# Optimization experiments

Measured on AMD Instinct MI355X. Metric: run time of the kernel, lower is better.

Reference implementation:

```python
import jax, jax.numpy as jnp
import numpy as np
from jax import lax

EPS = 1e-5  # torch LayerNorm / BatchNorm1d default eps
HEADS, DH, DEPTH, C = 4, 128, 2, 512


def setup_inputs() -> dict:
    key = jax.random.key(0)
    ks = iter(jax.random.split(key, 48))
    def rn(shape, scale=1.0):
        return jax.random.normal(next(ks), shape, jnp.float32) * scale
    d, L = 1024, DEPTH
    inp = {}
    inp['x'] = rn((16, 10, 256, d))                      # (b, ncrops, T, d)
    # Temporal embedding: Conv1d(d -> 512, k=3, pad=1) + ReLU
    inp['W_emb'] = rn((C, d, 3), (d * 3) ** -0.5)
    inp['b_emb'] = jnp.zeros((C,), jnp.float32)
    # Transformer (depth=2), params stacked along layer axis
    inp['ln1_g'] = jnp.ones((L, C), jnp.float32); inp['ln1_b'] = jnp.zeros((L, C), jnp.float32)
    inp['W_qkv'] = rn((L, C, 4 * HEADS * DH), C ** -0.5)  # to_qkv (no bias), inner_dim*4 = 2048
    inp['W_o']  = rn((L, 2 * HEADS * DH, C), (2 * HEADS * DH) ** -0.5)
    inp['b_o']  = jnp.zeros((L, C), jnp.float32)
    inp['ln2_g'] = jnp.ones((L, C), jnp.float32); inp['ln2_b'] = jnp.zeros((L, C), jnp.float32)
    inp['W_f1'] = rn((L, C, C), C ** -0.5); inp['b_f1'] = jnp.zeros((L, C), jnp.float32)
    inp['W_f2'] = rn((L, C, C), C ** -0.5); inp['b_f2'] = jnp.zeros((L, C), jnp.float32)
    # NormalHead: conv1 512->32 (k=1), bn1, conv2 32->16 (k=1), bn2, conv3 16->1 (k=1)
    inp['c1_W'] = rn((32, C), C ** -0.5); inp['c1_b'] = jnp.zeros((32,), jnp.float32)
    inp['bn1_g'] = jnp.ones((32,), jnp.float32); inp['bn1_b'] = jnp.zeros((32,), jnp.float32)
    inp['bn1_m'] = rn((32,), 0.1)
    inp['bn1_v'] = jax.random.uniform(next(ks), (32,), jnp.float32, 0.5, 1.5)
    inp['c2_W'] = rn((16, 32), 32 ** -0.5); inp['c2_b'] = jnp.zeros((16,), jnp.float32)
    inp['bn2_g'] = jnp.ones((16,), jnp.float32); inp['bn2_b'] = jnp.zeros((16,), jnp.float32)
    inp['bn2_m'] = rn((16,), 0.1)
    inp['bn2_v'] = jax.random.uniform(next(ks), (16,), jnp.float32, 0.5, 1.5)
    inp['c3_W'] = rn((1, 16), 0.25); inp['c3_b'] = jnp.zeros((1,), jnp.float32)
    return inp


def _ln(z, g, b):
    m = z.mean(-1, keepdims=True)
    v = ((z - m) ** 2).mean(-1, keepdims=True)
    return (z - m) / jnp.sqrt(v + EPS) * g + b


def _bn_eval(z, g, b, m, v):  # z: (B, C, T), eval-mode BatchNorm1d
    return (z - m[None, :, None]) / jnp.sqrt(v[None, :, None] + EPS) * g[None, :, None] + b[None, :, None]


def _k1conv(z, W, b):  # pointwise Conv1d: z (B, Ci, T), W (Co, Ci)
    return jnp.einsum('bct,oc->bot', z, W) + b[None, :, None]


def reference(x, W_emb, b_emb, ln1_g, ln1_b, W_qkv, W_o, b_o, ln2_g, ln2_b,
              W_f1, b_f1, W_f2, b_f2, c1_W, c1_b, bn1_g, bn1_b, bn1_m, bn1_v,
              c2_W, c2_b, bn2_g, bn2_b, bn2_m, bn2_v, c3_W, c3_b):
    b, n, T, d = x.shape
    h = x.reshape(b * n, T, d)
    # Temporal embedding: Conv1d(k=3, pad=1) + ReLU
    h = lax.conv_general_dilated(h.transpose(0, 2, 1), W_emb, (1,), 'SAME',
                                 dimension_numbers=('NCH', 'OIH', 'NCH'))
    h = jax.nn.relu(h + b_emb[None, :, None]).transpose(0, 2, 1)  # (BN, T, 512)

    # fixed positional-decay attention map attn2 (T, T), batch-independent
    idx = jnp.arange(T, dtype=jnp.float32)
    tg = jnp.abs(idx[None, :] - idx[:, None])
    a2 = jnp.exp(-tg / jnp.exp(1.0))
    a2 = a2 / a2.sum(-1)  # NOTE: broadcast over last axis, exactly as in the torch code

    scale = DH ** -0.5
    for l in range(DEPTH):
        z = _ln(h, ln1_g[l], ln1_b[l])
        qkvt = z @ W_qkv[l]                                   # (BN, T, 2048)
        q, k, v, t = jnp.split(qkvt, 4, axis=-1)
        def to_heads(u):
            return u.reshape(u.shape[0], T, HEADS, DH).transpose(0, 2, 1, 3)
        q, k, v, t = map(to_heads, (q, k, v, t))              # (BN, H, T, DH)
        attn1 = jax.nn.softmax(jnp.einsum('bhid,bhjd->bhij', q, k) * scale, axis=-1)
        o1 = jnp.einsum('bhij,bhjd->bhid', attn1, v)
        o2 = jnp.einsum('ij,bhjd->bhid', a2, t)
        o = jnp.concatenate([o1, o2], axis=-1)                # (BN, H, T, 2*DH)
        o = o.transpose(0, 2, 1, 3).reshape(h.shape[0], T, HEADS * 2 * DH)
        h = o @ W_o[l] + b_o[l] + h                           # attn residual
        z = _ln(h, ln2_g[l], ln2_b[l])
        h = (jax.nn.gelu(z @ W_f1[l] + b_f1[l], approximate=False) @ W_f2[l] + b_f2[l]) + h

    # NormalHead on (BN, C, T)
    f = h.transpose(0, 2, 1)
    x1 = _k1conv(f, c1_W, c1_b)                               # (BN, 32, T)
    x2 = _k1conv(jax.nn.relu(_bn_eval(x1, bn1_g, bn1_b, bn1_m, bn1_v)), c2_W, c2_b)  # (BN, 16, T)
    scores = jax.nn.sigmoid(_k1conv(jax.nn.relu(_bn_eval(x2, bn2_g, bn2_b, bn2_m, bn2_v)), c3_W, c3_b))
    normal_scores = scores.reshape(b, n, T).mean(1)           # mean over ncrops -> (b, T)

    def maha(feats, anchor, var):  # Mahalanobis distance vs BN running stats (no eps, as in source)
        dist = jnp.sqrt(jnp.sum((feats - anchor[None, :, None]) ** 2 / var[None, :, None], axis=1))
        return dist.reshape(b, n, T).mean(1)

    distance_sum = maha(x1, bn1_m, bn1_v) + maha(x2, bn2_m, bn2_v)
    return distance_sum * normal_scores                       # (b, T)
```

## Files before the change

kernel.cpp:

```cpp
#include <hip/hip_runtime.h>
#include <math.h>

#define T_    256
#define D_    1024
#define C_    512
#define H_    4
#define DH_   128
#define BNB   160
#define LEPS  1e-5f
#define INV_E 0.36787944117144233f
#define SCALE_ 0.08838834764831845f
#define LDT   40
#define XROW  264192

typedef unsigned short ushort;
typedef unsigned int   uint;
typedef __attribute__((ext_vector_type(8))) short short8;
typedef __attribute__((ext_vector_type(4))) float f32x4;

__device__ __forceinline__ ushort f2b(float f) {
    uint u = __float_as_uint(f);
    u += 0x7fffu + ((u >> 16) & 1u);
    return (ushort)(u >> 16);
}
__device__ __forceinline__ float b2f(ushort u) {
    return __uint_as_float(((uint)u) << 16);
}
__device__ __forceinline__ uint pk(float a, float b) {
    return (uint)f2b(a) | ((uint)f2b(b) << 16);
}
__device__ __forceinline__ void gl2lds(const void* g, void* l) {
    __builtin_amdgcn_global_load_lds(
        (const __attribute__((address_space(1))) void*)g,
        (__attribute__((address_space(3))) void*)l, 16, 0, 0);
}

__global__ void zero_k(float* __restrict__ p, int n) {
    int i = blockIdx.x * 256 + threadIdx.x;
    if (i < n) p[i] = 0.0f;
}

__global__ void xcvt_k(const float* __restrict__ src, ushort* __restrict__ dst, int n4) {
    int i = blockIdx.x * 256 + threadIdx.x;
    if (i < n4) {
        float4 f = ((const float4*)src)[i];
        uint2 v;
        v.x = pk(f.x, f.y);
        v.y = pk(f.z, f.w);
        int e   = i * 4;
        int bn  = e >> 18;
        int rem = e & 262143;
        ((uint2*)(dst + (size_t)bn * XROW + 1024 + rem))[0] = v;
    }
}

__global__ void xpad_k(ushort* __restrict__ dst, int nbn) {
    int i = blockIdx.x * 256 + threadIdx.x;
    if (i >= nbn * 1024) return;
    int bn = i >> 10, j = i & 1023;
    int r = j >> 9, c = j & 511;
    uint* base = (uint*)(dst + (size_t)bn * XROW);
    base[(r ? (XROW - 1024) / 2 : 0) + c] = 0u;
}

__global__ __launch_bounds__(256)
void tconv_k(const float* __restrict__ src, ushort* __restrict__ dst,
             int K, int N) {
    __shared__ float tile[32][33];
    int kb = blockIdx.x * 32, nb = blockIdx.y * 32;
    int tx = threadIdx.x & 31, ty = threadIdx.x >> 5;
#pragma unroll
    for (int i = 0; i < 32; i += 8)
        tile[ty + i][tx] = src[(size_t)(kb + ty + i) * N + nb + tx];
    __syncthreads();
#pragma unroll
    for (int i = 0; i < 32; i += 8)
        dst[(size_t)(nb + ty + i) * K + kb + tx] = f2b(tile[tx][ty + i]);
}

__global__ void bcvt_k(const float* __restrict__ src, ushort* __restrict__ dst, int n) {
    int i = blockIdx.x * 256 + threadIdx.x;
    if (i < n) dst[i] = f2b(src[i]);
}

__global__ void wemb_k(const float* __restrict__ W, ushort* __restrict__ Wt) {
    int idx = blockIdx.x * 256 + threadIdx.x;
    if (idx >= C_ * 3072) return;
    int c = idx / 3072, k = idx % 3072;
    int dt = k >> 10, ci = k & 1023;
    Wt[idx] = f2b(W[(size_t)c * 3072 + ci * 3 + dt]);
}

__global__ void a2_colsum_k(float* __restrict__ s) {
    int j = threadIdx.x;
    float acc = 0.0f;
    for (int k = 0; k < T_; k++) acc += expf(-fabsf((float)(j - k)) * INV_E);
    s[j] = acc;
}

__global__ void a2fill_k(const float* __restrict__ s, ushort* __restrict__ A2) {
    int i = blockIdx.x, j = threadIdx.x;
    A2[i * 256 + j] = f2b(expf(-fabsf((float)(i - j)) * INV_E) / s[j]);
}

__global__ __launch_bounds__(256)
void ln_k(const ushort* __restrict__ X, const float* __restrict__ g,
          const float* __restrict__ b, ushort* __restrict__ Z) {
    int row  = blockIdx.x * 4 + (threadIdx.x >> 6);
    int lane = threadIdx.x & 63;
    const ushort* xr = X + (size_t)row * C_ + lane * 8;
    uint4 raw = *(const uint4*)xr;
    float f[8];
    f[0] = __uint_as_float(raw.x << 16); f[1] = __uint_as_float(raw.x & 0xffff0000u);
    f[2] = __uint_as_float(raw.y << 16); f[3] = __uint_as_float(raw.y & 0xffff0000u);
    f[4] = __uint_as_float(raw.z << 16); f[5] = __uint_as_float(raw.z & 0xffff0000u);
    f[6] = __uint_as_float(raw.w << 16); f[7] = __uint_as_float(raw.w & 0xffff0000u);
    float s = 0.0f, s2 = 0.0f;
#pragma unroll
    for (int u = 0; u < 8; u++) { s += f[u]; s2 += f[u] * f[u]; }
#pragma unroll
    for (int m = 1; m < 64; m <<= 1) {
        s  += __shfl_xor(s, m);
        s2 += __shfl_xor(s2, m);
    }
    float mean = s * (1.0f / C_);
    float var  = s2 * (1.0f / C_) - mean * mean;
    float rinv = rsqrtf(var + LEPS);
    const float* gp = g + lane * 8;
    const float* bp = b + lane * 8;
    float4 g0 = *(const float4*)gp, g1 = *(const float4*)(gp + 4);
    float4 b0 = *(const float4*)bp, b1 = *(const float4*)(bp + 4);
    uint4 outv;
    outv.x = pk((f[0]-mean)*rinv*g0.x+b0.x, (f[1]-mean)*rinv*g0.y+b0.y);
    outv.y = pk((f[2]-mean)*rinv*g0.z+b0.z, (f[3]-mean)*rinv*g0.w+b0.w);
    outv.z = pk((f[4]-mean)*rinv*g1.x+b1.x, (f[5]-mean)*rinv*g1.y+b1.y);
    outv.w = pk((f[6]-mean)*rinv*g1.z+b1.z, (f[7]-mean)*rinv*g1.w+b1.w);
    *(uint4*)(Z + (size_t)row * C_ + lane * 8) = outv;
}


#define VMW_8 asm volatile("s_waitcnt vmcnt(8)" ::: "memory")
#define VMW_4 asm volatile("s_waitcnt vmcnt(4)" ::: "memory")
#define VMW_2 asm volatile("s_waitcnt vmcnt(2)" ::: "memory")
#define VMW_0 asm volatile("s_waitcnt vmcnt(0)" ::: "memory")
#define VMW_N
#define BAR() __builtin_amdgcn_s_barrier()
#define LGK0() do { asm volatile("s_waitcnt lgkmcnt(0)" ::: "memory"); \
                    __builtin_amdgcn_sched_barrier(0); } while (0)

#define TILE(kt, S1, S2, S3, S4, W1, W2, W4) do {                              \
                               \
    _Pragma("unroll") for (int mf = 0; mf < 4; mf++)                           \
      _Pragma("unroll") for (int ks = 0; ks < 2; ks++)                         \
        af[mf][ks] = ldA(kt, mf, ks);                                          \
    _Pragma("unroll") for (int nf = 0; nf < 2; nf++)                           \
      _Pragma("unroll") for (int ks = 0; ks < 2; ks++)                         \
        bf[nf][ks] = ldB(kt, nf, ks);                                          \
    if (S1) stageB((kt) + 1, 1);                                               \
    VMW_##W1; BAR(); LGK0();                                                   \
    __builtin_amdgcn_s_setprio(1);                                             \
    _Pragma("unroll") for (int ks = 0; ks < 2; ks++)                           \
      _Pragma("unroll") for (int mf = 0; mf < 4; mf++)                         \
        _Pragma("unroll") for (int nf = 0; nf < 2; nf++)                       \
          acc[mf][nf] = __builtin_amdgcn_mfma_f32_16x16x32_bf16(               \
              af[mf][ks], bf[nf][ks], acc[mf][nf], 0, 0, 0);                   \
    __builtin_amdgcn_s_setprio(0);                                             \
    BAR();                                                                     \
                \
    _Pragma("unroll") for (int nf = 2; nf < 4; nf++)                           \
      _Pragma("unroll") for (int ks = 0; ks < 2; ks++)                         \
        bf[nf][ks] = ldB(kt, nf, ks);                                          \
    if (S2) stageA((kt) + 1, 1);                                               \
    VMW_##W2; BAR(); LGK0();                                                   \
    __builtin_amdgcn_s_setprio(1);                                             \
    _Pragma("unroll") for (int ks = 0; ks < 2; ks++)                           \
      _Pragma("unroll") for (int mf = 0; mf < 4; mf++)                         \
        _Pragma("unroll") for (int nf = 2; nf < 4; nf++)                       \
          acc[mf][nf] = __builtin_amdgcn_mfma_f32_16x16x32_bf16(               \
              af[mf][ks], bf[nf][ks], acc[mf][nf], 0, 0, 0);                   \
    __builtin_amdgcn_s_setprio(0);                                             \
    BAR();                                                                     \
                               \
    _Pragma("unroll") for (int mf = 0; mf < 4; mf++)                           \
      _Pragma("unroll") for (int ks = 0; ks < 2; ks++)                         \
        af[mf][ks] = ldA(kt, mf + 4, ks);                                      \
    if (S3) stageA((kt) + 2, 0);                                               \
    BAR(); LGK0();                                                             \
    __builtin_amdgcn_s_setprio(1);                                             \
    _Pragma("unroll") for (int ks = 0; ks < 2; ks++)                           \
      _Pragma("unroll") for (int mf = 0; mf < 4; mf++)                         \
        _Pragma("unroll") for (int nf = 0; nf < 2; nf++)                       \
          acc[mf + 4][nf] = __builtin_amdgcn_mfma_f32_16x16x32_bf16(           \
              af[mf][ks], bf[nf][ks], acc[mf + 4][nf], 0, 0, 0);               \
    __builtin_amdgcn_s_setprio(0);                                             \
    BAR();                                                                     \
              \
    if (S4) stageB((kt) + 2, 0);                                               \
    VMW_##W4; BAR();                                                           \
    __builtin_amdgcn_s_setprio(1);                                             \
    _Pragma("unroll") for (int ks = 0; ks < 2; ks++)                           \
      _Pragma("unroll") for (int mf = 0; mf < 4; mf++)                         \
        _Pragma("unroll") for (int nf = 2; nf < 4; nf++)                       \
          acc[mf + 4][nf] = __builtin_amdgcn_mfma_f32_16x16x32_bf16(           \
              af[mf][ks], bf[nf][ks], acc[mf + 4][nf], 0, 0, 0);               \
    __builtin_amdgcn_s_setprio(0);                                             \
    BAR();                                                                     \
} while (0)

template<int CONV, int ACT, int RESID, int OUTBF>
__global__ __launch_bounds__(512, 2)
void gemm256_k(const ushort* __restrict__ A, const ushort* __restrict__ B,
               const float* __restrict__ bias, const ushort* __restrict__ R,
               void* __restrict__ Cout, int M, int N, int K,
               const ushort* __restrict__ Xp) {
    __shared__ __align__(16) ushort As[32768];
    __shared__ __align__(16) ushort Bs[32768];
    const int tid  = threadIdx.x;
    const int wave = tid >> 6, lane = tid & 63;
    const int wm = wave >> 2, wn = wave & 3;
    const int lm = lane & 15, quad = lane >> 4;

    const int NP = gridDim.x, My = gridDim.y;
    int m_idx, n_idx;
    if ((My & 7) == 0) {
        int bid = blockIdx.y * NP + blockIdx.x;
        m_idx = (bid & 7) + 8 * (bid / (8 * NP));
        n_idx = (bid >> 3) % NP;
    } else {
        m_idx = blockIdx.y; n_idx = blockIdx.x;
    }
    const int m0 = m_idx * 256, n0 = n_idx * 256;

    const int srow = lane >> 3;
    const int scol = ((lane & 7) ^ srow) << 3;

    auto stageA = [&](int kt, int half) {
        ushort* lds = As + (((kt & 1) * 2 + half) << 13) + (wave << 9);
        int r0 = half * 128 + wave * 8 + srow;
        if (CONV) {
            int k0 = kt << 6;
            int dt = k0 >> 10;
            int cb = (k0 & 1023) + scol;
            int g0 = m0 + r0;
            gl2lds(Xp + (size_t)(g0 >> 8) * XROW + ((g0 & 255) + dt) * 1024 + cb, lds);
            int g1 = g0 + 64;
            gl2lds(Xp + (size_t)(g1 >> 8) * XROW + ((g1 & 255) + dt) * 1024 + cb, lds + 4096);
        } else {
            const ushort* ga = A + (size_t)(m0 + r0) * K + (kt << 6) + scol;
            gl2lds(ga, lds);
            gl2lds(ga + (size_t)64 * K, lds + 4096);
        }
    };
    auto stageB = [&](int kt, int half) {
        ushort* lds = Bs + (((kt & 1) * 2 + half) << 13) + (wave << 9);
        const ushort* gb = B + (size_t)(n0 + half * 128 + wave * 8 + srow) * K
                             + (kt << 6) + scol;
        gl2lds(gb, lds);
        gl2lds(gb + (size_t)64 * K, lds + 4096);
    };

    auto ldA = [&](int kt, int mf, int ks) -> short8 {
        int r = wm * 16 + mf * 32 + lm;
        int slot = (quad + ks * 4) ^ (lm & 7);
        return *(const short8*)&As[(((kt & 1) * 2 + (r >> 7)) << 13)
                                   + (r & 127) * 64 + slot * 8];
    };
    auto ldB = [&](int kt, int nf, int ks) -> short8 {
        int r = wn * 16 + nf * 64 + lm;
        int slot = (quad + ks * 4) ^ (lm & 7);
        return *(const short8*)&Bs[(((kt & 1) * 2 + (r >> 7)) << 13)
                                   + (r & 127) * 64 + slot * 8];
    };

    short8 af[4][2], bf[4][2];
    f32x4 acc[8][4];
#pragma unroll
    for (int mf = 0; mf < 8; mf++)
#pragma unroll
        for (int nf = 0; nf < 4; nf++) acc[mf][nf] = (f32x4){0.f, 0.f, 0.f, 0.f};

    const int NT = K >> 6;
    stageA(0, 0); stageB(0, 0); stageB(0, 1); stageA(0, 1);
    stageA(1, 0); stageB(1, 0);
    VMW_8;
    BAR();

    for (int kt = 0; kt < NT - 2; kt++)
        TILE(kt, 1, 1, 1, 1, 8, 8, 8);
    TILE(NT - 2, 1, 1, 0, 0, 8, 8, 4);
    TILE(NT - 1, 0, 0, 0, 0, 2, 0, N);

#pragma unroll
    for (int mf = 0; mf < 8; mf++) {
        int grow0 = m0 + wm * 16 + mf * 32 + quad * 4;
#pragma unroll
        for (int nf = 0; nf < 4; nf++) {
            int gcol = n0 + wn * 16 + nf * 64 + lm;
            float bia = bias ? bias[gcol] : 0.0f;
            f32x4 v = acc[mf][nf];
#pragma unroll
            for (int i = 0; i < 4; i++) {
                int grow = grow0 + i;
                float val = v[i] + bia;
                if (ACT == 1) val = val * 0.5f * (1.0f + erff(val * 0.70710678118654752f));
                if (ACT == 2) val = fmaxf(val, 0.0f);
                if (RESID) val += b2f(R[(size_t)grow * N + gcol]);
                if (OUTBF) ((ushort*)Cout)[(size_t)grow * N + gcol] = f2b(val);
                else       ((float*)Cout)[(size_t)grow * N + gcol]  = val;
            }
        }
    }
}

__global__ __launch_bounds__(256)
void attn1_k(const ushort* __restrict__ qkvt, ushort* __restrict__ O) {
    const int bn = blockIdx.x, h = blockIdx.y;
    const int tid = threadIdx.x;
    const int wave = tid >> 6, lane = tid & 63;
    const int lm = lane & 15, quad = lane >> 4;
    __shared__ __align__(16) ushort Ks[32 * 136];
    __shared__ __align__(16) ushort Vt[128 * 40];
    __shared__ __align__(16) ushort Ps[4][64 * 40];
    const ushort* base = qkvt + (size_t)bn * T_ * 2048;

    short8 aq[4][4];
#pragma unroll
    for (int mt = 0; mt < 4; mt++) {
        const ushort* qrow = base + (size_t)(wave * 64 + mt * 16 + lm) * 2048 + h * DH_;
#pragma unroll
        for (int ks = 0; ks < 4; ks++)
            aq[mt][ks] = *(const short8*)(qrow + ks * 32 + quad * 8);
    }

    f32x4 oacc[4][8];
#pragma unroll
    for (int mt = 0; mt < 4; mt++)
#pragma unroll
        for (int nt = 0; nt < 8; nt++) oacc[mt][nt] = (f32x4){0.f, 0.f, 0.f, 0.f};
    float mrow[4][4], lrow[4][4];
#pragma unroll
    for (int mt = 0; mt < 4; mt++)
#pragma unroll
        for (int i = 0; i < 4; i++) { mrow[mt][i] = -1e30f; lrow[mt][i] = 0.0f; }

    for (int kt = 0; kt < 8; kt++) {
        __syncthreads();
#pragma unroll
        for (int u = 0; u < 2; u++) {
            int ii = tid + u * 256;
            int j = ii >> 4, dc = ii & 15;
            *(uint4*)&Ks[j * 136 + dc * 8] =
                *(const uint4*)(base + (size_t)(kt * 32 + j) * 2048 + 512 + h * DH_ + dc * 8);
        }
        {
            int j = tid & 31, half = tid >> 5;
            const ushort* vrow = base + (size_t)(kt * 32 + j) * 2048 + 1024 + h * DH_ + half * 16;
            uint4 v0 = *(const uint4*)vrow;
            uint4 v1 = *(const uint4*)(vrow + 8);
            ushort e[16];
            *(uint4*)&e[0] = v0; *(uint4*)&e[8] = v1;
#pragma unroll
            for (int u = 0; u < 16; u++)
                Vt[(half * 16 + u) * 40 + j] = e[u];
        }
        __syncthreads();

        f32x4 s[4][2];
#pragma unroll
        for (int mt = 0; mt < 4; mt++)
#pragma unroll
            for (int nt = 0; nt < 2; nt++) s[mt][nt] = (f32x4){0.f, 0.f, 0.f, 0.f};
#pragma unroll
        for (int ks = 0; ks < 4; ks++) {
            short8 bk0 = *(const short8*)&Ks[lm * 136 + ks * 32 + quad * 8];
            short8 bk1 = *(const short8*)&Ks[(16 + lm) * 136 + ks * 32 + quad * 8];
#pragma unroll
            for (int mt = 0; mt < 4; mt++) {
                s[mt][0] = __builtin_amdgcn_mfma_f32_16x16x32_bf16(aq[mt][ks], bk0, s[mt][0], 0, 0, 0);
                s[mt][1] = __builtin_amdgcn_mfma_f32_16x16x32_bf16(aq[mt][ks], bk1, s[mt][1], 0, 0, 0);
            }
        }

#pragma unroll
        for (int mt = 0; mt < 4; mt++) {
#pragma unroll
            for (int i = 0; i < 4; i++) {
                float v0 = s[mt][0][i] * SCALE_;
                float v1 = s[mt][1][i] * SCALE_;
                float rmax = fmaxf(v0, v1);
#pragma unroll
                for (int mk = 1; mk < 16; mk <<= 1)
                    rmax = fmaxf(rmax, __shfl_xor(rmax, mk));
                float mold = mrow[mt][i];
                float mnew = fmaxf(mold, rmax);
                float alpha = __expf(mold - mnew);
                float p0 = __expf(v0 - mnew);
                float p1 = __expf(v1 - mnew);
                float rs = p0 + p1;
#pragma unroll
                for (int mk = 1; mk < 16; mk <<= 1)
                    rs += __shfl_xor(rs, mk);
                lrow[mt][i] = lrow[mt][i] * alpha + rs;
                mrow[mt][i] = mnew;
#pragma unroll
                for (int nt = 0; nt < 8; nt++) {
                    oacc[mt][nt][i] *= alpha;
                }
                int prow = mt * 16 + quad * 4 + i;
                Ps[wave][prow * 40 + lm]      = f2b(p0);
                Ps[wave][prow * 40 + 16 + lm] = f2b(p1);
            }
        }

        short8 ap[4];
#pragma unroll
        for (int mt = 0; mt < 4; mt++)
            ap[mt] = *(const short8*)&Ps[wave][(mt * 16 + lm) * 40 + quad * 8];
#pragma unroll
        for (int nt = 0; nt < 8; nt++) {
            short8 bv = *(const short8*)&Vt[(nt * 16 + lm) * 40 + quad * 8];
#pragma unroll
            for (int mt = 0; mt < 4; mt++)
                oacc[mt][nt] = __builtin_amdgcn_mfma_f32_16x16x32_bf16(ap[mt], bv, oacc[mt][nt], 0, 0, 0);
        }
    }

#pragma unroll
    for (int mt = 0; mt < 4; mt++) {
#pragma unroll
        for (int i = 0; i < 4; i++) {
            int row = wave * 64 + mt * 16 + quad * 4 + i;
            float rinv = 1.0f / lrow[mt][i];
#pragma unroll
            for (int nt = 0; nt < 8; nt++) {
                int d = nt * 16 + lm;
                O[((size_t)bn * T_ + row) * 1024 + h * 256 + d] =
                    f2b(oacc[mt][nt][i] * rinv);
            }
        }
    }
}

__global__ __launch_bounds__(256)
void attn2_k(const ushort* __restrict__ A2, const ushort* __restrict__ qkvt,
             ushort* __restrict__ O) {
    __shared__ __align__(16) ushort As[128 * LDT];
    __shared__ __align__(16) ushort Bs[128 * 48];
    const int tid = threadIdx.x;
    const int bn = blockIdx.z;
    const int m0 = blockIdx.y * 128;
    const int n0 = blockIdx.x * 128;
    const int lane = tid & 63, wave = tid >> 6;
    const int wr = wave >> 1, wc = wave & 1;
    const int lm = lane & 15, quad = lane >> 4;
    const ushort* tbase = qkvt + (size_t)bn * T_ * 2048 + 1536;
    const int r = tid >> 1, c0 = (tid & 1) * 2;

    f32x4 acc[4][4];
#pragma unroll
    for (int mt = 0; mt < 4; mt++)
#pragma unroll
        for (int nt = 0; nt < 4; nt++) acc[mt][nt] = (f32x4){0.f, 0.f, 0.f, 0.f};

    for (int k0 = 0; k0 < 256; k0 += 32) {
        const ushort* Arow = A2 + (size_t)(m0 + r) * 256 + k0;
        *(uint4*)&As[r * LDT + c0 * 8]       = *(const uint4*)(Arow + c0 * 8);
        *(uint4*)&As[r * LDT + (c0 + 1) * 8] = *(const uint4*)(Arow + (c0 + 1) * 8);
        {
            int kr = tid & 31, np = tid >> 5;
            const ushort* trow = tbase + (size_t)(k0 + kr) * 2048 + n0 + np * 16;
            uint4 v0 = *(const uint4*)trow;
            uint4 v1 = *(const uint4*)(trow + 8);
            ushort e[16];
            *(uint4*)&e[0] = v0; *(uint4*)&e[8] = v1;
#pragma unroll
            for (int u = 0; u < 16; u++)
                Bs[(np * 16 + u) * 48 + kr] = e[u];
        }
        __syncthreads();
        short8 af[4], bf[4];
#pragma unroll
        for (int mt = 0; mt < 4; mt++)
            af[mt] = *(const short8*)&As[(wr * 64 + mt * 16 + lm) * LDT + quad * 8];
#pragma unroll
        for (int nt = 0; nt < 4; nt++)
            bf[nt] = *(const short8*)&Bs[(wc * 64 + nt * 16 + lm) * 48 + quad * 8];
#pragma unroll
        for (int mt = 0; mt < 4; mt++)
#pragma unroll
            for (int nt = 0; nt < 4; nt++)
                acc[mt][nt] = __builtin_amdgcn_mfma_f32_16x16x32_bf16(
                    af[mt], bf[nt], acc[mt][nt], 0, 0, 0);
        __syncthreads();
    }

#pragma unroll
    for (int mt = 0; mt < 4; mt++) {
        int row0 = m0 + wr * 64 + mt * 16 + quad * 4;
#pragma unroll
        for (int nt = 0; nt < 4; nt++) {
            int n = n0 + wc * 64 + nt * 16 + lm;
            int h = n >> 7, d = n & 127;
#pragma unroll
            for (int i = 0; i < 4; i++) {
                int row = row0 + i;
                O[((size_t)bn * T_ + row) * 1024 + h * 256 + 128 + d] =
                    f2b(acc[mt][nt][i]);
            }
        }
    }
}

#define BLD 520
__global__ __launch_bounds__(256)
void head1_k(const ushort* __restrict__ Hb, const ushort* __restrict__ c1Wb,
             const float* __restrict__ c1b, float* __restrict__ X1) {
    __shared__ __align__(16) ushort As[128 * LDT];
    __shared__ __align__(16) ushort Bs[32 * BLD];
    const int tid = threadIdx.x;
    const int lane = tid & 63, wave = tid >> 6;
    const int lm = lane & 15, quad = lane >> 4;
    const int m0 = blockIdx.x * 128;
#pragma unroll
    for (int u = 0; u < 8; u++) {
        int ii = tid + u * 256;
        int nrow = ii >> 6;
        int koff = (ii & 63) * 8;
        *(uint4*)&Bs[nrow * BLD + koff] = *(const uint4*)(c1Wb + nrow * 512 + koff);
    }
    f32x4 acc[2][2];
#pragma unroll
    for (int mt = 0; mt < 2; mt++)
#pragma unroll
        for (int nt = 0; nt < 2; nt++) acc[mt][nt] = (f32x4){0.f, 0.f, 0.f, 0.f};

    const int r = tid >> 1, half = tid & 1;
    for (int k0 = 0; k0 < 512; k0 += 32) {
        const ushort* s = Hb + (size_t)(m0 + r) * 512 + k0 + half * 16;
        uint4 v0 = *(const uint4*)s;
        uint4 v1 = *(const uint4*)(s + 8);
        __syncthreads();
        *(uint4*)&As[r * LDT + half * 16]     = v0;
        *(uint4*)&As[r * LDT + half * 16 + 8] = v1;
        __syncthreads();
        short8 af[2], bf[2];
#pragma unroll
        for (int mt = 0; mt < 2; mt++)
            af[mt] = *(const short8*)&As[(wave * 32 + mt * 16 + lm) * LDT + quad * 8];
#pragma unroll
        for (int nt = 0; nt < 2; nt++)
            bf[nt] = *(const short8*)&Bs[(nt * 16 + lm) * BLD + k0 + quad * 8];
#pragma unroll
        for (int mt = 0; mt < 2; mt++)
#pragma unroll
            for (int nt = 0; nt < 2; nt++)
                acc[mt][nt] = __builtin_amdgcn_mfma_f32_16x16x32_bf16(
                    af[mt], bf[nt], acc[mt][nt], 0, 0, 0);
    }
#pragma unroll
    for (int mt = 0; mt < 2; mt++) {
        int row0 = m0 + wave * 32 + mt * 16 + quad * 4;
#pragma unroll
        for (int nt = 0; nt < 2; nt++) {
            int col = nt * 16 + lm;
            float bia = c1b[col];
#pragma unroll
            for (int i = 0; i < 4; i++)
                X1[(size_t)(row0 + i) * 32 + col] = acc[mt][nt][i] + bia;
        }
    }
}

__global__ __launch_bounds__(256)
void head2_k(const float* __restrict__ X1, int bn_base, int M,
             const float* __restrict__ g1, const float* __restrict__ b1,
             const float* __restrict__ m1, const float* __restrict__ v1,
             const float* __restrict__ c2W, const float* __restrict__ c2b,
             const float* __restrict__ g2, const float* __restrict__ b2,
             const float* __restrict__ m2, const float* __restrict__ v2,
             const float* __restrict__ c3W, const float* __restrict__ c3b,
             float* __restrict__ sum_dist, float* __restrict__ sum_score) {
    int row = blockIdx.x * 256 + threadIdx.x;
    if (row >= M) return;
    float x1[32], y1[32];
    const float* xr = X1 + (size_t)row * 32;
#pragma unroll
    for (int c = 0; c < 32; c++) x1[c] = xr[c];
    float d1 = 0.0f;
#pragma unroll
    for (int c = 0; c < 32; c++) {
        float dd = x1[c] - m1[c];
        d1 += dd * dd / v1[c];
        y1[c] = fmaxf(0.0f, dd * rsqrtf(v1[c] + LEPS) * g1[c] + b1[c]);
    }
    float d2 = 0.0f, sc = c3b[0];
#pragma unroll
    for (int o = 0; o < 16; o++) {
        float acc = c2b[o];
        const float* wr = c2W + o * 32;
#pragma unroll
        for (int c = 0; c < 32; c++) acc += wr[c] * y1[c];
        float dd = acc - m2[o];
        d2 += dd * dd / v2[o];
        float y2 = fmaxf(0.0f, dd * rsqrtf(v2[o] + LEPS) * g2[o] + b2[o]);
        sc += c3W[o] * y2;
    }
    float dist = sqrtf(d1) + sqrtf(d2);
    sc = 1.0f / (1.0f + expf(-sc));
    int bn = bn_base + (row >> 8);
    int t = row & 255;
    int b = bn / 10;
    atomicAdd(&sum_dist[b * T_ + t], dist);
    atomicAdd(&sum_score[b * T_ + t], sc);
}

__global__ void combine_k(const float* __restrict__ sd, const float* __restrict__ ss,
                          float* __restrict__ out) {
    int i = blockIdx.x * 256 + threadIdx.x;
    if (i < 16 * T_) out[i] = (sd[i] * 0.1f) * (ss[i] * 0.1f);
}

extern "C" void kernel_launch(void* const* d_in, const int* in_sizes, int n_in,
                              void* d_out, int out_size, void* d_ws, size_t ws_size,
                              hipStream_t stream) {
    const float* x     = (const float*)d_in[0];
    const float* W_emb = (const float*)d_in[1];
    const float* b_emb = (const float*)d_in[2];
    const float* ln1_g = (const float*)d_in[3];
    const float* ln1_b = (const float*)d_in[4];
    const float* W_qkv = (const float*)d_in[5];
    const float* W_o   = (const float*)d_in[6];
    const float* b_o   = (const float*)d_in[7];
    const float* ln2_g = (const float*)d_in[8];
    const float* ln2_b = (const float*)d_in[9];
    const float* W_f1  = (const float*)d_in[10];
    const float* b_f1  = (const float*)d_in[11];
    const float* W_f2  = (const float*)d_in[12];
    const float* b_f2  = (const float*)d_in[13];
    const float* c1_W  = (const float*)d_in[14];
    const float* c1_b  = (const float*)d_in[15];
    const float* bn1_g = (const float*)d_in[16];
    const float* bn1_b = (const float*)d_in[17];
    const float* bn1_m = (const float*)d_in[18];
    const float* bn1_v = (const float*)d_in[19];
    const float* c2_W  = (const float*)d_in[20];
    const float* c2_b  = (const float*)d_in[21];
    const float* bn2_g = (const float*)d_in[22];
    const float* bn2_b = (const float*)d_in[23];
    const float* bn2_m = (const float*)d_in[24];
    const float* bn2_v = (const float*)d_in[25];
    const float* c3_W  = (const float*)d_in[26];
    const float* c3_b  = (const float*)d_in[27];
    float* out = (float*)d_out;

    char* p = (char*)d_ws;
    auto alloc = [&](size_t bytes) -> char* {
        char* q = p; p += (bytes + 255) & ~(size_t)255; return q;
    };
    ushort* wEmb = (ushort*)alloc((size_t)C_ * 3072 * 2);
    ushort* wQkv = (ushort*)alloc((size_t)2 * 2048 * 512 * 2);
    ushort* wO   = (ushort*)alloc((size_t)2 * 512 * 1024 * 2);
    ushort* wF1  = (ushort*)alloc((size_t)2 * 512 * 512 * 2);
    ushort* wF2  = (ushort*)alloc((size_t)2 * 512 * 512 * 2);
    ushort* A2bf = (ushort*)alloc((size_t)256 * 256 * 2);
    ushort* c1Wb = (ushort*)alloc((size_t)32 * 512 * 2);
    float*  s256      = (float*)alloc(256 * 4);
    float*  sum_dist  = (float*)alloc(4096 * 4);
    float*  sum_score = (float*)alloc(4096 * 4);
    size_t fixedB = (size_t)(p - (char*)d_ws);

    int CH = 8;
    const int cands[7] = {160, 80, 40, 32, 20, 16, 10};
    for (int ci = 0; ci < 7; ci++) {
        size_t per = (size_t)cands[ci] * 256 * 10384 + 16384;
        if (fixedB + per <= ws_size) { CH = cands[ci]; break; }
    }
    const int MR = CH * 256;
    ushort* xbp  = (ushort*)alloc((size_t)CH * XROW * 2);
    ushort* h    = (ushort*)alloc((size_t)MR * 512 * 2);
    ushort* z    = (ushort*)alloc((size_t)MR * 512 * 2);
    ushort* qkvt = (ushort*)alloc((size_t)MR * 2048 * 2);
    ushort* o    = (ushort*)alloc((size_t)MR * 1024 * 2);
    ushort* g    = o;
    float*  X1   = (float*)alloc((size_t)MR * 32 * 4);

    zero_k<<<(8192 + 255) / 256, 256, 0, stream>>>(sum_dist, 8192);
    a2_colsum_k<<<1, 256, 0, stream>>>(s256);
    a2fill_k<<<256, 256, 0, stream>>>(s256, A2bf);
    wemb_k<<<(C_ * 3072 + 255) / 256, 256, 0, stream>>>(W_emb, wEmb);
    bcvt_k<<<(32 * 512 + 255) / 256, 256, 0, stream>>>(c1_W, c1Wb, 32 * 512);
    for (int l = 0; l < 2; l++) {
        tconv_k<<<dim3(512 / 32, 2048 / 32), 256, 0, stream>>>(
            W_qkv + (size_t)l * 512 * 2048, wQkv + (size_t)l * 2048 * 512, 512, 2048);
        tconv_k<<<dim3(1024 / 32, 512 / 32), 256, 0, stream>>>(
            W_o + (size_t)l * 1024 * 512, wO + (size_t)l * 512 * 1024, 1024, 512);
        tconv_k<<<dim3(512 / 32, 512 / 32), 256, 0, stream>>>(
            W_f1 + (size_t)l * 512 * 512, wF1 + (size_t)l * 512 * 512, 512, 512);
        tconv_k<<<dim3(512 / 32, 512 / 32), 256, 0, stream>>>(
            W_f2 + (size_t)l * 512 * 512, wF2 + (size_t)l * 512 * 512, 512, 512);
    }

    for (int cs = 0; cs < BNB; cs += CH) {
        const float* xc = x + (size_t)cs * T_ * D_;

        int n4 = MR * 1024 / 4;
        xcvt_k<<<(n4 + 255) / 256, 256, 0, stream>>>(xc, xbp, n4);
        xpad_k<<<(CH * 1024 + 255) / 256, 256, 0, stream>>>(xbp, CH);

        gemm256_k<1, 2, 0, 1><<<dim3(512 / 256, MR / 256), 512, 0, stream>>>(
            nullptr, wEmb, b_emb, nullptr, h, MR, 512, 3072, xbp);

        for (int l = 0; l < 2; l++) {
            ln_k<<<MR / 4, 256, 0, stream>>>(h, ln1_g + l * C_, ln1_b + l * C_, z);
            gemm256_k<0, 0, 0, 1><<<dim3(2048 / 256, MR / 256), 512, 0, stream>>>(
                z, wQkv + (size_t)l * 2048 * 512, nullptr, nullptr, qkvt,
                MR, 2048, 512, nullptr);
            attn1_k<<<dim3(CH, H_), 256, 0, stream>>>(qkvt, o);
            attn2_k<<<dim3(4, 2, CH), 256, 0, stream>>>(A2bf, qkvt, o);
            gemm256_k<0, 0, 1, 1><<<dim3(512 / 256, MR / 256), 512, 0, stream>>>(
                o, wO + (size_t)l * 512 * 1024, b_o + l * C_, h, h,
                MR, 512, 1024, nullptr);
            ln_k<<<MR / 4, 256, 0, stream>>>(h, ln2_g + l * C_, ln2_b + l * C_, z);
            gemm256_k<0, 1, 0, 1><<<dim3(512 / 256, MR / 256), 512, 0, stream>>>(
                z, wF1 + (size_t)l * 512 * 512, b_f1 + l * C_, nullptr, g,
                MR, 512, 512, nullptr);
            gemm256_k<0, 0, 1, 1><<<dim3(512 / 256, MR / 256), 512, 0, stream>>>(
                g, wF2 + (size_t)l * 512 * 512, b_f2 + l * C_, h, h,
                MR, 512, 512, nullptr);
        }

        head1_k<<<MR / 128, 256, 0, stream>>>(h, c1Wb, c1_b, X1);
        head2_k<<<MR / 256, 256, 0, stream>>>(
            X1, cs, MR, bn1_g, bn1_b, bn1_m, bn1_v,
            c2_W, c2_b, bn2_g, bn2_b, bn2_m, bn2_v, c3_W, c3_b,
            sum_dist, sum_score);
    }

    combine_k<<<16, 256, 0, stream>>>(sum_dist, sum_score, out);
}
```

Baseline: 1.677 ms.

## Deepen gemm256 prefetch pipeline and use 128-tile GEMM for N=512 layers

Reworks the 256x256 GEMM main loop so both halves of the next-next K tile are staged earlier, and B fragments for the next tile are preloaded. Barriers are removed from the first two phases, and LDS waits are partial (lgkmcnt 4). The goal is to hide global-to-LDS latency better. It also adds a simpler 128x128 GEMM kernel and uses it for the N=512 projection and FFN GEMMs, which raises block count and occupancy for those narrow outputs. The cost is a simple single-buffered loop with two syncthreads per 32-wide K step in the new kernel, plus tighter wait-count logic that risks hazards.

```diff
diff --git a/kernel.cpp b/kernel.cpp
--- a/kernel.cpp
+++ b/kernel.cpp
@@ -139,25 +139,28 @@
 }
 
 
-#define VMW_8 asm volatile("s_waitcnt vmcnt(8)" ::: "memory")
-#define VMW_4 asm volatile("s_waitcnt vmcnt(4)" ::: "memory")
-#define VMW_2 asm volatile("s_waitcnt vmcnt(2)" ::: "memory")
-#define VMW_0 asm volatile("s_waitcnt vmcnt(0)" ::: "memory")
+#define VMW_12 asm volatile("s_waitcnt vmcnt(12)" ::: "memory")
+#define VMW_10 asm volatile("s_waitcnt vmcnt(10)" ::: "memory")
+#define VMW_8  asm volatile("s_waitcnt vmcnt(8)"  ::: "memory")
+#define VMW_4  asm volatile("s_waitcnt vmcnt(4)"  ::: "memory")
+#define VMW_2  asm volatile("s_waitcnt vmcnt(2)"  ::: "memory")
+#define VMW_0  asm volatile("s_waitcnt vmcnt(0)"  ::: "memory")
 #define VMW_N
 #define BAR() __builtin_amdgcn_s_barrier()
-#define LGK0() do { asm volatile("s_waitcnt lgkmcnt(0)" ::: "memory"); \
-                    __builtin_amdgcn_sched_barrier(0); } while (0)
-
-#define TILE(kt, S1, S2, S3, S4, W1, W2, W4) do {                              \
-                               \
+#define LGK4 do { asm volatile("s_waitcnt lgkmcnt(4)" ::: "memory"); \
+                  __builtin_amdgcn_sched_barrier(0); } while (0)
+#define LGK0 do { asm volatile("s_waitcnt lgkmcnt(0)" ::: "memory"); \
+                  __builtin_amdgcn_sched_barrier(0); } while (0)
+
+#define TILE(kt, S, W2, W3, W4, R4) do {                                       \
+              \
     _Pragma("unroll") for (int mf = 0; mf < 4; mf++)                           \
       _Pragma("unroll") for (int ks = 0; ks < 2; ks++)                         \
         af[mf][ks] = ldA(kt, mf, ks);                                          \
-    _Pragma("unroll") for (int nf = 0; nf < 2; nf++)                           \
+    _Pragma("unroll") for (int nf = 2; nf < 4; nf++)                           \
       _Pragma("unroll") for (int ks = 0; ks < 2; ks++)                         \
         bf[nf][ks] = ldB(kt, nf, ks);                                          \
-    if (S1) stageB((kt) + 1, 1);                                               \
-    VMW_##W1; BAR(); LGK0();                                                   \
+    LGK4;                                                                      \
     __builtin_amdgcn_s_setprio(1);                                             \
     _Pragma("unroll") for (int ks = 0; ks < 2; ks++)                           \
       _Pragma("unroll") for (int mf = 0; mf < 4; mf++)                         \
@@ -166,12 +169,9 @@
               af[mf][ks], bf[nf][ks], acc[mf][nf], 0, 0, 0);                   \
     __builtin_amdgcn_s_setprio(0);                                             \
     BAR();                                                                     \
-                \
-    _Pragma("unroll") for (int nf = 2; nf < 4; nf++)                           \
-      _Pragma("unroll") for (int ks = 0; ks < 2; ks++)                         \
-        bf[nf][ks] = ldB(kt, nf, ks);                                          \
-    if (S2) stageA((kt) + 1, 1);                                               \
-    VMW_##W2; BAR(); LGK0();                                                   \
+              \
+    if (S) { stageA((kt) + 2, 0); stageB((kt) + 2, 0); }                       \
+    LGK0;                                                                      \
     __builtin_amdgcn_s_setprio(1);                                             \
     _Pragma("unroll") for (int ks = 0; ks < 2; ks++)                           \
       _Pragma("unroll") for (int mf = 0; mf < 4; mf++)                         \
@@ -179,13 +179,13 @@
           acc[mf][nf] = __builtin_amdgcn_mfma_f32_16x16x32_bf16(               \
               af[mf][ks], bf[nf][ks], acc[mf][nf], 0, 0, 0);                   \
     __builtin_amdgcn_s_setprio(0);                                             \
-    BAR();                                                                     \
-                               \
+    VMW_##W2; BAR();                                                           \
+       \
+    if (S) stageB((kt) + 2, 1);                                                \
     _Pragma("unroll") for (int mf = 0; mf < 4; mf++)                           \
       _Pragma("unroll") for (int ks = 0; ks < 2; ks++)                         \
         af[mf][ks] = ldA(kt, mf + 4, ks);                                      \
-    if (S3) stageA((kt) + 2, 0);                                               \
-    BAR(); LGK0();                                                             \
+    LGK0;                                                                      \
     __builtin_amdgcn_s_setprio(1);                                             \
     _Pragma("unroll") for (int ks = 0; ks < 2; ks++)                           \
       _Pragma("unroll") for (int mf = 0; mf < 4; mf++)                         \
@@ -193,10 +193,13 @@
           acc[mf + 4][nf] = __builtin_amdgcn_mfma_f32_16x16x32_bf16(           \
               af[mf][ks], bf[nf][ks], acc[mf + 4][nf], 0, 0, 0);               \
     __builtin_amdgcn_s_setprio(0);                                             \
-    BAR();                                                                     \
-              \
-    if (S4) stageB((kt) + 2, 0);                                               \
-    VMW_##W4; BAR();                                                           \
+    VMW_##W3; BAR();                                                           \
+     \
+    if (S) stageA((kt) + 2, 1);                                                \
+    if (R4)                                                                    \
+      _Pragma("unroll") for (int nf = 0; nf < 2; nf++)                         \
+        _Pragma("unroll") for (int ks = 0; ks < 2; ks++)                       \
+          bf[nf][ks] = ldB((kt) + 1, nf, ks);                                  \
     __builtin_amdgcn_s_setprio(1);                                             \
     _Pragma("unroll") for (int ks = 0; ks < 2; ks++)                           \
       _Pragma("unroll") for (int mf = 0; mf < 4; mf++)                         \
@@ -204,7 +207,7 @@
           acc[mf + 4][nf] = __builtin_amdgcn_mfma_f32_16x16x32_bf16(           \
               af[mf][ks], bf[nf][ks], acc[mf + 4][nf], 0, 0, 0);               \
     __builtin_amdgcn_s_setprio(0);                                             \
-    BAR();                                                                     \
+    VMW_##W4; BAR();                                                           \
 } while (0)
 
 template<int CONV, int ACT, int RESID, int OUTBF>
@@ -281,14 +284,18 @@
 
     const int NT = K >> 6;
     stageA(0, 0); stageB(0, 0); stageB(0, 1); stageA(0, 1);
-    stageA(1, 0); stageB(1, 0);
-    VMW_8;
+    stageA(1, 0); stageB(1, 0); stageB(1, 1); stageA(1, 1);
+    VMW_10;
     BAR();
+#pragma unroll
+    for (int nf = 0; nf < 2; nf++)
+#pragma unroll
+        for (int ks = 0; ks < 2; ks++) bf[nf][ks] = ldB(0, nf, ks);
 
     for (int kt = 0; kt < NT - 2; kt++)
-        TILE(kt, 1, 1, 1, 1, 8, 8, 8);
-    TILE(NT - 2, 1, 1, 0, 0, 8, 8, 4);
-    TILE(NT - 1, 0, 0, 0, 0, 2, 0, N);
+        TILE(kt, 1, 12, 10, 10, 1);
+    TILE(NT - 2, 0, 8, 4, 2, 1);
+    TILE(NT - 1, 0, 0, N, N, 0);
 
 #pragma unroll
     for (int mf = 0; mf < 8; mf++) {
@@ -298,6 +305,100 @@
             int gcol = n0 + wn * 16 + nf * 64 + lm;
             float bia = bias ? bias[gcol] : 0.0f;
             f32x4 v = acc[mf][nf];
+#pragma unroll
+            for (int i = 0; i < 4; i++) {
+                int grow = grow0 + i;
+                float val = v[i] + bia;
+                if (ACT == 1) val = val * 0.5f * (1.0f + erff(val * 0.70710678118654752f));
+                if (ACT == 2) val = fmaxf(val, 0.0f);
+                if (RESID) val += b2f(R[(size_t)grow * N + gcol]);
+                if (OUTBF) ((ushort*)Cout)[(size_t)grow * N + gcol] = f2b(val);
+                else       ((float*)Cout)[(size_t)grow * N + gcol]  = val;
+            }
+        }
+    }
+}
+
+template<int CONV, int ACT, int RESID, int OUTBF>
+__global__ __launch_bounds__(256)
+void gemm_k(const ushort* __restrict__ A, const ushort* __restrict__ B,
+            const float* __restrict__ bias, const ushort* __restrict__ R,
+            void* __restrict__ Cout, int M, int N, int K,
+            const ushort* __restrict__ Xp) {
+    __shared__ __align__(16) ushort As[128 * 32];
+    __shared__ __align__(16) ushort Bs[128 * 32];
+    const int tid  = threadIdx.x;
+    const int lane = tid & 63, wave = tid >> 6;
+    const int wr = wave >> 1, wc = wave & 1;
+    const int lm = lane & 15, quad = lane >> 4;
+
+    const int NP = gridDim.x, My = gridDim.y;
+    int m_idx, n_idx;
+    if ((My & 7) == 0) {
+        int bid = blockIdx.y * NP + blockIdx.x;
+        m_idx = (bid & 7) + 8 * (bid / (8 * NP));
+        n_idx = (bid >> 3) % NP;
+    } else {
+        m_idx = blockIdx.y; n_idx = blockIdx.x;
+    }
+    const int m0 = m_idx * 128, n0 = n_idx * 128;
+
+    const int srow   = lane >> 2;
+    const int schunk = (lane & 3) * 8;
+    ushort* AsW = As + wave * 32 * 32;
+    ushort* BsW = Bs + wave * 32 * 32;
+
+    f32x4 acc[4][4];
+#pragma unroll
+    for (int mt = 0; mt < 4; mt++)
+#pragma unroll
+        for (int nt = 0; nt < 4; nt++) acc[mt][nt] = (f32x4){0.f, 0.f, 0.f, 0.f};
+
+    for (int k0 = 0; k0 < K; k0 += 32) {
+        if (CONV) {
+            int dt = k0 >> 10;
+            int ci = (k0 & 1023) + schunk;
+            int g0 = m0 + wave * 32 + srow;
+            int bn0 = g0 >> 8, t0 = g0 & 255;
+            int g1 = g0 + 16;
+            int bn1 = g1 >> 8, t1 = g1 & 255;
+            gl2lds(Xp + (size_t)bn0 * XROW + (t0 + dt) * 1024 + ci, AsW);
+            gl2lds(Xp + (size_t)bn1 * XROW + (t1 + dt) * 1024 + ci, AsW + 16 * 32);
+        } else {
+            const ushort* ga = A + (size_t)(m0 + wave * 32 + srow) * K + k0 + schunk;
+            gl2lds(ga, AsW);
+            gl2lds(ga + (size_t)16 * K, AsW + 16 * 32);
+        }
+        {
+            const ushort* gb = B + (size_t)(n0 + wave * 32 + srow) * K + k0 + schunk;
+            gl2lds(gb, BsW);
+            gl2lds(gb + (size_t)16 * K, BsW + 16 * 32);
+        }
+        __syncthreads();
+        short8 af[4], bfv[4];
+#pragma unroll
+        for (int mt = 0; mt < 4; mt++)
+            af[mt] = *(const short8*)&As[(wr * 64 + mt * 16 + lm) * 32 + quad * 8];
+#pragma unroll
+        for (int nt = 0; nt < 4; nt++)
+            bfv[nt] = *(const short8*)&Bs[(wc * 64 + nt * 16 + lm) * 32 + quad * 8];
+#pragma unroll
+        for (int mt = 0; mt < 4; mt++)
+#pragma unroll
+            for (int nt = 0; nt < 4; nt++)
+                acc[mt][nt] = __builtin_amdgcn_mfma_f32_16x16x32_bf16(
+                    af[mt], bfv[nt], acc[mt][nt], 0, 0, 0);
+        __syncthreads();
+    }
+
+#pragma unroll
+    for (int mt = 0; mt < 4; mt++) {
+        int grow0 = m0 + wr * 64 + mt * 16 + quad * 4;
+#pragma unroll
+        for (int nt = 0; nt < 4; nt++) {
+            int gcol = n0 + wc * 64 + nt * 16 + lm;
+            float bia = bias ? bias[gcol] : 0.0f;
+            f32x4 v = acc[mt][nt];
 #pragma unroll
             for (int i = 0; i < 4; i++) {
                 int grow = grow0 + i;
@@ -717,14 +818,14 @@
                 MR, 2048, 512, nullptr);
             attn1_k<<<dim3(CH, H_), 256, 0, stream>>>(qkvt, o);
             attn2_k<<<dim3(4, 2, CH), 256, 0, stream>>>(A2bf, qkvt, o);
-            gemm256_k<0, 0, 1, 1><<<dim3(512 / 256, MR / 256), 512, 0, stream>>>(
+            gemm_k<0, 0, 1, 1><<<dim3(512 / 128, MR / 128), 256, 0, stream>>>(
                 o, wO + (size_t)l * 512 * 1024, b_o + l * C_, h, h,
                 MR, 512, 1024, nullptr);
             ln_k<<<MR / 4, 256, 0, stream>>>(h, ln2_g + l * C_, ln2_b + l * C_, z);
-            gemm256_k<0, 1, 0, 1><<<dim3(512 / 256, MR / 256), 512, 0, stream>>>(
+            gemm_k<0, 1, 0, 1><<<dim3(512 / 128, MR / 128), 256, 0, stream>>>(
                 z, wF1 + (size_t)l * 512 * 512, b_f1 + l * C_, nullptr, g,
                 MR, 512, 512, nullptr);
-            gemm256_k<0, 0, 1, 1><<<dim3(512 / 256, MR / 256), 512, 0, stream>>>(
+            gemm_k<0, 0, 1, 1><<<dim3(512 / 128, MR / 128), 256, 0, stream>>>(
                 g, wF2 + (size_t)l * 512 * 512, b_f2 + l * C_, h, h,
                 MR, 512, 512, nullptr);
         }
```

Result: slower. 1.763 ms (+5.1%).
